# Kernel optimization log

Measured on AMD Instinct MI355X. Metric: run time of the kernel, lower is better.

Reference implementation:

```python
import jax, jax.numpy as jnp
import numpy as np
import math

B, T, D = 2, 2048, 1024
H, HD = 16, 64          # num_heads, head_dim = D // H
ROPE, BASE = 64, 10000.0  # rope covers full head dim
GLOBAL_IDS = jnp.array([2, 3, 4, 5, 6, 7], dtype=jnp.int32)


def setup_inputs() -> dict:
    key = jax.random.key(0)
    k1, k2, k3, k4 = jax.random.split(key, 4)
    x = jax.random.normal(k1, (B, T, D), dtype=jnp.float32)
    input_ids = jax.random.randint(k2, (B, T), 0, 1024, dtype=jnp.int32)
    W_qkv = jax.random.normal(k3, (3 * H * HD, D), dtype=jnp.float32) * 0.02
    b_qkv = jnp.zeros((3 * H * HD,), dtype=jnp.float32)
    W_out = jax.random.normal(k4, (D, H * HD), dtype=jnp.float32) * 0.02
    b_out = jnp.zeros((D,), dtype=jnp.float32)
    return {"x": x, "input_ids": input_ids, "W_qkv": W_qkv, "b_qkv": b_qkv,
            "W_out": W_out, "b_out": b_out}


def _apply_rotary(x, cos, sin):
    # x: [B,H,T,HD]; rope covers first ROPE dims (= full head here)
    x_rot, x_pass = x[..., :ROPE], x[..., ROPE:]
    half = ROPE // 2
    x1, x2 = x_rot[..., :half], x_rot[..., half:]
    x1n = x1 * cos - x2 * sin
    x2n = x1 * sin + x2 * cos
    return jnp.concatenate([x1n, x2n, x_pass], axis=-1)


def reference(x, input_ids, W_qkv, b_qkv, W_out, b_out):
    Bx, Tx, _ = x.shape
    qkv = x @ W_qkv.T + b_qkv                      # [B,T,3*H*HD]
    q, k, v = jnp.split(qkv, 3, axis=-1)
    def heads(t):
        return t.reshape(Bx, Tx, H, HD).transpose(0, 2, 1, 3)  # [B,H,T,HD]
    q, k, v = heads(q), heads(k), heads(v)

    # RoPE
    pos = jnp.arange(Tx, dtype=jnp.float32)
    inv_freq = 1.0 / (BASE ** (jnp.arange(0, ROPE, 2, dtype=jnp.float32) / ROPE))
    freqs = pos[:, None] * inv_freq[None, :]        # [T, ROPE//2]
    cos, sin = jnp.cos(freqs)[None, None], jnp.sin(freqs)[None, None]
    q = _apply_rotary(q, cos, sin)
    k = _apply_rotary(k, cos, sin)

    # causal mask OR global-query rows (BigBird-style)
    causal = jnp.tril(jnp.ones((Tx, Tx), dtype=bool))[None, None]   # [1,1,T,T]
    global_mask = jnp.isin(input_ids, GLOBAL_IDS)                    # [B,T]
    allow = causal | global_mask[:, None, :, None]                   # [B,1,T,T]

    scale = math.sqrt(HD)
    logits = jnp.einsum('bhqd,bhkd->bhqk', q, k) / scale
    neg = -jnp.finfo(logits.dtype).max
    logits = jnp.where(allow, logits, neg)
    attn = jax.nn.softmax(logits, axis=-1)
    out = jnp.einsum('bhqk,bhkd->bhqd', attn, v)
    out = out.transpose(0, 2, 1, 3).reshape(Bx, Tx, H * HD)
    return out @ W_out.T + b_out
```

## Files before the change

### kernel.cpp

```cpp
#include <hip/hip_runtime.h>
#include <math.h>

#define Bc 2
#define Tc 2048
#define Dc 1024
#define Hc 16
#define HDc 64

typedef __attribute__((ext_vector_type(8))) short bf16x8;
typedef __attribute__((ext_vector_type(4))) float f32x4;
typedef __attribute__((ext_vector_type(16))) float f32x16;

__device__ __forceinline__ unsigned short f2bf(float f) {
    union { float f; unsigned int u; } v; v.f = f;
    unsigned int r = (v.u + 0x7FFFu + ((v.u >> 16) & 1u)) >> 16;
    return (unsigned short)r;
}
__device__ __forceinline__ unsigned pack2bf(float a, float b) {
    unsigned au = __float_as_uint(a) + 0x8000u;
    unsigned bu = __float_as_uint(b) + 0x8000u;
    return __builtin_amdgcn_perm(bu, au, 0x07060302u);
}

__device__ __forceinline__ void gload_lds16(const unsigned short* g,
                                            unsigned short* l) {
    __builtin_amdgcn_global_load_lds(
        (const __attribute__((address_space(1))) unsigned int*)g,
        (__attribute__((address_space(3))) unsigned int*)l,
        16, 0, 0);
}

#define CEXP 0.1803368801111204f

__global__ __launch_bounds__(256) void convert_bf16(
    const float* __restrict__ x, const float* __restrict__ wqkv,
    const float* __restrict__ wout,
    unsigned short* __restrict__ xb, unsigned short* __restrict__ wqkvb,
    unsigned short* __restrict__ woutb, float2* __restrict__ ropeTab)
{
    const int gid = blockIdx.x * 256 + threadIdx.x;
    if (gid < Tc * 32) {
        const int t = gid >> 5, i = gid & 31;
        const float freq = exp2f((float)i * -0.4152410118609203f);
        const float ang = (float)t * freq;
        ropeTab[gid] = make_float2(cosf(ang), sinf(ang));
    }
    const int i = gid * 4;
    const float* src; unsigned short* dst; int off;
    if (i < 4194304)      { src = x;    dst = xb;    off = i; }
    else if (i < 7340032) { src = wqkv; dst = wqkvb; off = i - 4194304; }
    else                  { src = wout; dst = woutb; off = i - 7340032; }
    float4 v = *(const float4*)&src[off];
    ushort4 o;
    o.x = f2bf(v.x); o.y = f2bf(v.y); o.z = f2bf(v.z); o.w = f2bf(v.w);
    *(ushort4*)&dst[off] = o;
}

template <int MODE>
__global__ __launch_bounds__(256) void gemm_mfma(
    const unsigned short* __restrict__ A, const unsigned short* __restrict__ W,
    const float* __restrict__ bias, float* __restrict__ C,
    unsigned short* __restrict__ Qp, unsigned short* __restrict__ Kp,
    unsigned short* __restrict__ Vtp, const float2* __restrict__ ropeTab,
    int M, int N, int K)
{
    __shared__ unsigned short Apk[128 * 8 * 8];
    __shared__ unsigned short Bpk[128 * 8 * 8];

    const int tid = threadIdx.x;
    const int lane = tid & 63;
    const int wave = tid >> 6;
    const int quad = lane >> 4;
    const int c = lane & 15;
    const int wm = wave >> 1;
    const int wn = wave & 1;
    const int m0 = blockIdx.y * 128;
    const int n0 = blockIdx.x * 128;

    f32x4 acc[4][4];
#pragma unroll
    for (int mt = 0; mt < 4; mt++)
#pragma unroll
        for (int nt = 0; nt < 4; nt++) acc[mt][nt] = (f32x4){0.f, 0.f, 0.f, 0.f};

    const int lrow = lane >> 3;
    const int srcoct = (lane & 7) ^ lrow;

    for (int k0 = 0; k0 < K; k0 += 64) {
        __syncthreads();
#pragma unroll
        for (int i = 0; i < 4; i++) {
            const int r = wave * 32 + i * 8 + lrow;
            gload_lds16(&A[(size_t)(m0 + r) * K + k0 + srcoct * 8],
                        &Apk[(wave * 32 + i * 8) * 64]);
            gload_lds16(&W[(size_t)(n0 + r) * K + k0 + srcoct * 8],
                        &Bpk[(wave * 32 + i * 8) * 64]);
        }
        __syncthreads();
#pragma unroll
        for (int ko = 0; ko < 2; ko++) {
            bf16x8 af[4], bf[4];
#pragma unroll
            for (int mt = 0; mt < 4; mt++) {
                const int m = wm * 64 + mt * 16 + c;
                af[mt] = *(const bf16x8*)&Apk[(m * 8 + ((ko * 4 + quad) ^ (m & 7))) * 8];
            }
#pragma unroll
            for (int nt = 0; nt < 4; nt++) {
                const int n = wn * 64 + nt * 16 + c;
                bf[nt] = *(const bf16x8*)&Bpk[(n * 8 + ((ko * 4 + quad) ^ (n & 7))) * 8];
            }
#pragma unroll
            for (int mt = 0; mt < 4; mt++)
#pragma unroll
                for (int nt = 0; nt < 4; nt++)
                    acc[mt][nt] = __builtin_amdgcn_mfma_f32_16x16x32_bf16(
                        af[mt], bf[nt], acc[mt][nt], 0, 0, 0);
        }
    }

    if (MODE == 0) {
#pragma unroll
        for (int mt = 0; mt < 4; mt++) {
            const int m = m0 + wm * 64 + mt * 16 + quad * 4;
#pragma unroll
            for (int nt = 0; nt < 4; nt++) {
                const int n = n0 + wn * 64 + nt * 16 + c;
                const float bv = bias[n];
#pragma unroll
                for (int reg = 0; reg < 4; reg++)
                    C[(size_t)(m + reg) * N + n] = acc[mt][nt][reg] + bv;
            }
        }
    } else {
        const int n_wave = n0 + wn * 64;
        const int which = n_wave >> 10;
        const int h = (n_wave >> 6) & 15;
        const int b = m0 >> 11;
        const int t_base = (m0 & 2047) + wm * 64;

        __syncthreads();
        unsigned short* stg = ((wave < 2) ? Apk : Bpk) + (wave & 1) * 4096;

        if (which < 2) {
            unsigned short* dst = (which == 0) ? Qp : Kp;
#pragma unroll
            for (int mt = 0; mt < 4; mt++) {
#pragma unroll
                for (int nt = 0; nt < 2; nt++) {
                    const int i1 = nt * 16 + c;
                    const float bv1 = bias[n_wave + i1];
                    const float bv2 = bias[n_wave + 32 + i1];
#pragma unroll
                    for (int reg = 0; reg < 4; reg++) {
                        const int row = mt * 16 + quad * 4 + reg;
                        const float2 cs = ropeTab[(t_base + row) * 32 + i1];
                        const float x1 = acc[mt][nt][reg] + bv1;
                        const float x2 = acc[mt][nt + 2][reg] + bv2;
                        const int col2 = 32 + i1;
                        stg[(row * 8 + ((i1 >> 3) ^ (row & 7))) * 8 + (i1 & 7)] =
                            f2bf(x1 * cs.x - x2 * cs.y);
                        stg[(row * 8 + ((col2 >> 3) ^ (row & 7))) * 8 + (col2 & 7)] =
                            f2bf(x1 * cs.y + x2 * cs.x);
                    }
                }
            }
            const size_t obase = ((size_t)(b * Hc + h) * Tc + t_base) * HDc;
            const int oct = lane & 7;
#pragma unroll
            for (int k = 0; k < 8; k++) {
                const int f = lane * 8 + k * 512;
                const int row = f >> 6;
                bf16x8 vv = *(const bf16x8*)&stg[(row * 8 + (oct ^ (row & 7))) * 8];
                *(bf16x8*)&dst[obase + f] = vv;
            }
        } else {
#pragma unroll
            for (int mt = 0; mt < 4; mt++) {
#pragma unroll
                for (int nt = 0; nt < 4; nt++) {
                    const int d = nt * 16 + c;
                    const float bv = bias[n_wave + d];
#pragma unroll
                    for (int reg = 0; reg < 4; reg++) {
                        const int r = mt * 16 + quad * 4 + reg;
                        stg[(d * 8 + ((r >> 3) ^ (d & 7))) * 8 + (r & 7)] =
                            f2bf(acc[mt][nt][reg] + bv);
                    }
                }
            }
            const size_t vbase = (size_t)(b * Hc + h) * HDc * Tc;
            const int oct = lane & 7;
#pragma unroll
            for (int k = 0; k < 8; k++) {
                const int d = (lane >> 3) + k * 8;
                bf16x8 vv = *(const bf16x8*)&stg[(d * 8 + (oct ^ (d & 7))) * 8];
                *(bf16x8*)&Vtp[vbase + (size_t)d * Tc + t_base + oct * 8] = vv;
            }
        }
    }
}

__global__ __launch_bounds__(256) void attn_fused(
    const unsigned short* __restrict__ Q, const unsigned short* __restrict__ K,
    const unsigned short* __restrict__ Vt, const int* __restrict__ ids,
    unsigned short* __restrict__ AO)
{
    __shared__ float smem[8448];

    const int tid = threadIdx.x;
    const int lane = tid & 63;
    const int wave = tid >> 6;
    const int c32 = lane & 31;
    const int h = lane >> 5;
    const int blk = blockIdx.x;

    if (blk < 32) {
        int* s_list = (int*)smem;
        int* s_cnt = (int*)smem + 64;
        float* s_accm = smem + 128;
        float* s_lm = s_accm + 8192;

        const int bh = blk;
        const int b = bh >> 4;
        const int hd = bh & 15;
        const size_t qkbase = (size_t)bh * Tc * HDc;

        if (tid == 0) *s_cnt = 0;
        __syncthreads();
        for (int i = tid; i < Tc; i += 256) {
            int id = ids[b * Tc + i];
            if ((unsigned)(id - 2) <= 5u) {
                int p = atomicAdd(s_cnt, 1);
                if (p < 64) s_list[p] = i;
            }
        }
        __syncthreads();
        const int cnt = min(*s_cnt, 64);

        for (int pass = 0; pass * 32 < cnt; pass++) {
            const int slot = pass * 32 + c32;
            const int row = (slot < cnt) ? s_list[slot] : s_list[0];

            bf16x8 qf[4];
#pragma unroll
            for (int ko = 0; ko < 4; ko++)
                qf[ko] = *(const bf16x8*)&Q[qkbase + (size_t)row * HDc + ko * 16 + h * 8];

            f32x16 acc0 = {}, acc1 = {};
            float lacc = 0.0f;

            for (int it = wave; it < Tc / 64; it += 4) {
                const int t0 = it * 64;
                f32x16 s0 = {}, s1 = {};
#pragma unroll
                for (int ko = 0; ko < 4; ko++) {
                    const int koff = ko * 16 + h * 8;
                    bf16x8 kf0 = *(const bf16x8*)&K[qkbase + (size_t)(t0 + c32) * HDc + koff];
                    bf16x8 kf1 = *(const bf16x8*)&K[qkbase + (size_t)(t0 + 32 + c32) * HDc + koff];
                    s0 = __builtin_amdgcn_mfma_f32_32x32x16_bf16(kf0, qf[ko], s0, 0, 0, 0);
                    s1 = __builtin_amdgcn_mfma_f32_32x32x16_bf16(kf1, qf[ko], s1, 0, 0, 0);
                }
                float v[32];
#pragma unroll
                for (int r = 0; r < 16; r++) { v[r] = s0[r]; v[16 + r] = s1[r]; }
#pragma unroll
                for (int i = 0; i < 32; i++) v[i] = exp2f(v[i] * CEXP);
                unsigned pk[16];
#pragma unroll
                for (int i = 0; i < 16; i++) pk[i] = pack2bf(v[2 * i], v[2 * i + 1]);
#pragma unroll
                for (int st = 1; st < 32; st <<= 1)
#pragma unroll
                    for (int i = 0; i < 32; i += 2 * st) v[i] += v[i + st];
                lacc += v[0];
#pragma unroll
                for (int ko = 0; ko < 4; ko++) {
                    const int a = (ko >> 1) * 8 + (ko & 1) * 4;
                    unsigned keep0 = h ? pk[a + 2] : pk[a + 0];
                    unsigned keep1 = h ? pk[a + 3] : pk[a + 1];
                    unsigned send0 = h ? pk[a + 0] : pk[a + 2];
                    unsigned send1 = h ? pk[a + 1] : pk[a + 3];
                    unsigned recv0 = (unsigned)__shfl_xor((int)send0, 32);
                    unsigned recv1 = (unsigned)__shfl_xor((int)send1, 32);
                    union { bf16x8 v8; unsigned u[4]; } pf;
                    pf.u[0] = h ? recv0 : keep0;
                    pf.u[1] = h ? recv1 : keep1;
                    pf.u[2] = h ? keep0 : recv0;
                    pf.u[3] = h ? keep1 : recv1;
                    const int oct = ko * 2 + h;
                    bf16x8 vf0 = *(const bf16x8*)&Vt[qkbase + (size_t)c32 * Tc + t0 + oct * 8];
                    bf16x8 vf1 = *(const bf16x8*)&Vt[qkbase + (size_t)(32 + c32) * Tc + t0 + oct * 8];
                    acc0 = __builtin_amdgcn_mfma_f32_32x32x16_bf16(vf0, pf.v8, acc0, 0, 0, 0);
                    acc1 = __builtin_amdgcn_mfma_f32_32x32x16_bf16(vf1, pf.v8, acc1, 0, 0, 0);
                }
            }

            const float lfull = lacc + __shfl_xor(lacc, 32);
            if (h == 0) s_lm[wave * 32 + c32] = lfull;
#pragma unroll
            for (int r = 0; r < 16; r++) {
                const int d = (r & 3) + 8 * (r >> 2) + 4 * h;
                s_accm[(wave * 64 + d) * 32 + c32] = acc0[r];
                s_accm[(wave * 64 + 32 + d) * 32 + c32] = acc1[r];
            }
            __syncthreads();
            for (int i = tid; i < 2048; i += 256) {
                const int sl = i >> 6, d = i & 63;
                if (pass * 32 + sl < cnt) {
                    const float o = s_accm[(0 * 64 + d) * 32 + sl] + s_accm[(1 * 64 + d) * 32 + sl] +
                                    s_accm[(2 * 64 + d) * 32 + sl] + s_accm[(3 * 64 + d) * 32 + sl];
                    const float lt = s_lm[sl] + s_lm[32 + sl] + s_lm[64 + sl] + s_lm[96 + sl];
                    const int qrow = s_list[pass * 32 + sl];
                    AO[((size_t)(b * Tc + qrow)) * Dc + hd * HDc + d] = f2bf(o / lt);
                }
            }
            __syncthreads();
        }
        return;
    }

    unsigned short* KV = (unsigned short*)smem;

    const int idx = blk - 32;
    const int bh = idx & 31;
    const int b = bh >> 4;
    const int hd = bh & 15;
    const int qb = 15 - (idx >> 5);
    const int qb0 = qb * 128;
    const int wq0 = qb0 + wave * 32;
    const size_t qkbase = (size_t)bh * Tc * HDc;
    const int q = wq0 + c32;

    bf16x8 qf[4];
#pragma unroll
    for (int ko = 0; ko < 4; ko++)
        qf[ko] = *(const bf16x8*)&Q[qkbase + (size_t)q * HDc + ko * 16 + h * 8];

    const int myid = ids[b * Tc + q];
    const bool gr = ((unsigned)(myid - 2) <= 5u);

    f32x16 acc0 = {}, acc1 = {};
    float lacc = 0.0f;

    const int nIter = 2 * qb + 2;
    const int skey = tid >> 3;
    const int soct = tid & 7;

    bf16x8 kA0, kA1, vA0, vA1, kB0, kB1, vB0, vB1;

    auto loadT = [&](int t0, bf16x8& k0, bf16x8& k1, bf16x8& v0, bf16x8& v1) {
        const int r0 = skey, r1 = skey + 32;
        k0 = *(const bf16x8*)&K[qkbase + (size_t)(t0 + r0) * HDc + soct * 8];
        k1 = *(const bf16x8*)&K[qkbase + (size_t)(t0 + r1) * HDc + soct * 8];
        v0 = *(const bf16x8*)&Vt[qkbase + (size_t)r0 * Tc + t0 + soct * 8];
        v1 = *(const bf16x8*)&Vt[qkbase + (size_t)r1 * Tc + t0 + soct * 8];
    };
    auto writeT = [&](int buf, bf16x8 k0, bf16x8 k1, bf16x8 v0, bf16x8 v1) {
        const int r0 = skey, r1 = skey + 32;
        unsigned short* Kb = KV + buf * 4096;
        unsigned short* Vb = KV + 8192 + buf * 4096;
        *(bf16x8*)&Kb[(r0 * 8 + (soct ^ (r0 & 7))) * 8] = k0;
        *(bf16x8*)&Kb[(r1 * 8 + (soct ^ (r1 & 7))) * 8] = k1;
        *(bf16x8*)&Vb[(r0 * 8 + (soct ^ (r0 & 7))) * 8] = v0;
        *(bf16x8*)&Vb[(r1 * 8 + (soct ^ (r1 & 7))) * 8] = v1;
    };

    auto compute = [&](int buf, int t0) {
        if (t0 > wq0 + 31) return;
        const unsigned short* Kb = KV + buf * 4096;
        const unsigned short* Vb = KV + 8192 + buf * 4096;

        f32x16 s0 = {}, s1 = {};
#pragma unroll
        for (int ko = 0; ko < 4; ko++) {
            const int oct = ko * 2 + h;
            const int k0i = c32;
            const int k1i = 32 + c32;
            bf16x8 kf0 = *(const bf16x8*)&Kb[(k0i * 8 + (oct ^ (k0i & 7))) * 8];
            bf16x8 kf1 = *(const bf16x8*)&Kb[(k1i * 8 + (oct ^ (k1i & 7))) * 8];
            s0 = __builtin_amdgcn_mfma_f32_32x32x16_bf16(kf0, qf[ko], s0, 0, 0, 0);
            s1 = __builtin_amdgcn_mfma_f32_32x32x16_bf16(kf1, qf[ko], s1, 0, 0, 0);
        }

        float v[32];
#pragma unroll
        for (int r = 0; r < 16; r++) { v[r] = s0[r]; v[16 + r] = s1[r]; }
#pragma unroll
        for (int i = 0; i < 32; i++) v[i] = exp2f(v[i] * CEXP);

        const bool needMask = (t0 + 63 > wq0);
        if (needMask) {
            const int thr = wq0 + c32 - t0 - 4 * h;
#pragma unroll
            for (int kt = 0; kt < 2; kt++)
#pragma unroll
                for (int r = 0; r < 16; r++) {
                    const int ckr = kt * 32 + (r & 3) + 8 * (r >> 2);
                    v[kt * 16 + r] = (ckr <= thr) ? v[kt * 16 + r] : 0.0f;
                }
        }

        unsigned pk[16];
#pragma unroll
        for (int i = 0; i < 16; i++) pk[i] = pack2bf(v[2 * i], v[2 * i + 1]);

#pragma unroll
        for (int st = 1; st < 32; st <<= 1)
#pragma unroll
            for (int i = 0; i < 32; i += 2 * st) v[i] += v[i + st];
        lacc += v[0];

#pragma unroll
        for (int ko = 0; ko < 4; ko++) {
            const int a = (ko >> 1) * 8 + (ko & 1) * 4;
            unsigned keep0 = h ? pk[a + 2] : pk[a + 0];
            unsigned keep1 = h ? pk[a + 3] : pk[a + 1];
            unsigned send0 = h ? pk[a + 0] : pk[a + 2];
            unsigned send1 = h ? pk[a + 1] : pk[a + 3];
            unsigned recv0 = (unsigned)__shfl_xor((int)send0, 32);
            unsigned recv1 = (unsigned)__shfl_xor((int)send1, 32);
            union { bf16x8 v8; unsigned u[4]; } pf;
            pf.u[0] = h ? recv0 : keep0;
            pf.u[1] = h ? recv1 : keep1;
            pf.u[2] = h ? keep0 : recv0;
            pf.u[3] = h ? keep1 : recv1;
            const int oct = ko * 2 + h;
            const int d0 = c32, d1 = 32 + c32;
            bf16x8 vf0 = *(const bf16x8*)&Vb[(d0 * 8 + (oct ^ (d0 & 7))) * 8];
            bf16x8 vf1 = *(const bf16x8*)&Vb[(d1 * 8 + (oct ^ (d1 & 7))) * 8];
            acc0 = __builtin_amdgcn_mfma_f32_32x32x16_bf16(vf0, pf.v8, acc0, 0, 0, 0);
            acc1 = __builtin_amdgcn_mfma_f32_32x32x16_bf16(vf1, pf.v8, acc1, 0, 0, 0);
        }
    };

    loadT(0, kA0, kA1, vA0, vA1);
    writeT(0, kA0, kA1, vA0, vA1);
    for (int it = 0; ; it += 2) {
        __syncthreads();
        const bool p1 = (it + 1) < nIter;
        if (p1) loadT((it + 1) * 64, kB0, kB1, vB0, vB1);
        compute(0, it * 64);
        if (!p1) break;
        writeT(1, kB0, kB1, vB0, vB1);
        __syncthreads();
        const bool p2 = (it + 2) < nIter;
        if (p2) loadT((it + 2) * 64, kA0, kA1, vA0, vA1);
        compute(1, (it + 1) * 64);
        if (!p2) break;
        writeT(0, kA0, kA1, vA0, vA1);
    }

    const float l = lacc + __shfl_xor(lacc, 32);
    if (!gr) {
        const float inv = 1.0f / l;
        unsigned short* dst = &AO[((size_t)(b * Tc + q)) * Dc + hd * HDc];
#pragma unroll
        for (int i = 0; i < 8; i++) {
            const int r = 2 * i;
            const int d = (r & 3) + 8 * (r >> 2) + 4 * h;
            *(unsigned*)&dst[d]      = pack2bf(acc0[r] * inv, acc0[r + 1] * inv);
            *(unsigned*)&dst[32 + d] = pack2bf(acc1[r] * inv, acc1[r + 1] * inv);
        }
    }
}

extern "C" void kernel_launch(void* const* d_in, const int* in_sizes, int n_in,
                              void* d_out, int out_size, void* d_ws, size_t ws_size,
                              hipStream_t stream)
{
    const float* x    = (const float*)d_in[0];
    const int*   ids  = (const int*)d_in[1];
    const float* Wqkv = (const float*)d_in[2];
    const float* bqkv = (const float*)d_in[3];
    const float* Wout = (const float*)d_in[4];
    const float* bout = (const float*)d_in[5];
    float* out = (float*)d_out;

    const size_t TEN = (size_t)Bc * Hc * Tc * HDc;
    unsigned short* xb    = (unsigned short*)d_ws;
    unsigned short* wqkvb = xb + 4194304;
    unsigned short* woutb = wqkvb + 3145728;
    float2* ropeTab       = (float2*)(woutb + 1048576);
    unsigned short* Qb    = (unsigned short*)(ropeTab + 65536);
    unsigned short* Kb    = Qb + TEN;
    unsigned short* Vtb   = Kb + TEN;
    unsigned short* AOb   = Vtb + TEN;

    convert_bf16<<<8192, 256, 0, stream>>>(x, Wqkv, Wout, xb, wqkvb, woutb,
                                           ropeTab);
    dim3 g1(3072 / 128, 4096 / 128);
    gemm_mfma<1><<<g1, 256, 0, stream>>>(xb, wqkvb, bqkv, nullptr,
                                         Qb, Kb, Vtb, ropeTab, 4096, 3072, 1024);
    attn_fused<<<544, 256, 0, stream>>>(Qb, Kb, Vtb, ids, AOb);
    dim3 g4(1024 / 128, 4096 / 128);
    gemm_mfma<0><<<g4, 256, 0, stream>>>(AOb, woutb, bout, out,
                                         nullptr, nullptr, nullptr, nullptr,
                                         4096, 1024, 1024);
}
```

Measured before the change: 202.7 us.

## Split attention into 64-row query blocks with key-split wave pairs and direct LDS loads

The causal attention grid now uses 64-row query blocks instead of 128, giving 1024 blocks, ordered to interleave long and short blocks for load balance. Within each block two wave pairs process alternate key tiles, and their partial accumulators are merged through shared memory at the end. K/V staging switches from register loads followed by LDS writes to direct global-to-LDS loads, and launch bounds request 4 blocks per CU. The cost is an extra merge step, the loss of overlap between loading and computing within a block, and register pressure from the occupancy hint.

Result: no change. 200.7 us (-1.0%).

```diff
diff --git a/kernel.cpp b/kernel.cpp
--- a/kernel.cpp
+++ b/kernel.cpp
@@ -201,12 +201,12 @@
     }
 }
 
-__global__ __launch_bounds__(256) void attn_fused(
+__global__ __launch_bounds__(256, 4) void attn_fused(
     const unsigned short* __restrict__ Q, const unsigned short* __restrict__ K,
     const unsigned short* __restrict__ Vt, const int* __restrict__ ids,
     unsigned short* __restrict__ AO)
 {
-    __shared__ float smem[8448];
+    __shared__ __align__(16) float smem[8448];
 
     const int tid = threadIdx.x;
     const int lane = tid & 63;
@@ -321,14 +321,21 @@
     }
 
     unsigned short* KV = (unsigned short*)smem;
+    unsigned short* Ke = KV;
+    unsigned short* Ko = KV + 4096;
+    unsigned short* Ve = KV + 8192;
+    unsigned short* Vo = KV + 12288;
 
     const int idx = blk - 32;
-    const int bh = idx & 31;
+    const int bh = (idx & 7) + 8 * ((idx >> 3) & 3);
     const int b = bh >> 4;
     const int hd = bh & 15;
-    const int qb = 15 - (idx >> 5);
-    const int qb0 = qb * 128;
-    const int wq0 = qb0 + wave * 32;
+    const int w = idx >> 5;
+    const int u = w & 7, tq = w >> 3;
+    const int j = (tq == 0) ? u : (tq == 1) ? 31 - u : (tq == 2) ? 8 + u : 23 - u;
+    const int qb0 = j * 64;
+    const int nT = j + 1;
+    const int wq0 = qb0 + (wave & 1) * 32;
     const size_t qkbase = (size_t)bh * Tc * HDc;
     const int q = wq0 + c32;
 
@@ -343,34 +350,30 @@
     f32x16 acc0 = {}, acc1 = {};
     float lacc = 0.0f;
 
-    const int nIter = 2 * qb + 2;
-    const int skey = tid >> 3;
-    const int soct = tid & 7;
-
-    bf16x8 kA0, kA1, vA0, vA1, kB0, kB1, vB0, vB1;
-
-    auto loadT = [&](int t0, bf16x8& k0, bf16x8& k1, bf16x8& v0, bf16x8& v1) {
-        const int r0 = skey, r1 = skey + 32;
-        k0 = *(const bf16x8*)&K[qkbase + (size_t)(t0 + r0) * HDc + soct * 8];
-        k1 = *(const bf16x8*)&K[qkbase + (size_t)(t0 + r1) * HDc + soct * 8];
-        v0 = *(const bf16x8*)&Vt[qkbase + (size_t)r0 * Tc + t0 + soct * 8];
-        v1 = *(const bf16x8*)&Vt[qkbase + (size_t)r1 * Tc + t0 + soct * 8];
+    const int lrow = lane >> 3;
+    const int srcoct = (lane & 7) ^ lrow;
+    const int jb = wave * 2;
+
+    auto stageK = [&](int t0, unsigned short* buf) {
+#pragma unroll
+        for (int i = 0; i < 2; i++) {
+            const int jj = jb + i;
+            const int row = jj * 8 + lrow;
+            gload_lds16(&K[qkbase + (size_t)(t0 + row) * HDc + srcoct * 8],
+                        &buf[jj * 512]);
+        }
     };
-    auto writeT = [&](int buf, bf16x8 k0, bf16x8 k1, bf16x8 v0, bf16x8 v1) {
-        const int r0 = skey, r1 = skey + 32;
-        unsigned short* Kb = KV + buf * 4096;
-        unsigned short* Vb = KV + 8192 + buf * 4096;
-        *(bf16x8*)&Kb[(r0 * 8 + (soct ^ (r0 & 7))) * 8] = k0;
-        *(bf16x8*)&Kb[(r1 * 8 + (soct ^ (r1 & 7))) * 8] = k1;
-        *(bf16x8*)&Vb[(r0 * 8 + (soct ^ (r0 & 7))) * 8] = v0;
-        *(bf16x8*)&Vb[(r1 * 8 + (soct ^ (r1 & 7))) * 8] = v1;
+    auto stageV = [&](int t0, unsigned short* buf) {
+#pragma unroll
+        for (int i = 0; i < 2; i++) {
+            const int jj = jb + i;
+            const int d = jj * 8 + lrow;
+            gload_lds16(&Vt[qkbase + (size_t)d * Tc + t0 + srcoct * 8],
+                        &buf[jj * 512]);
+        }
     };
 
-    auto compute = [&](int buf, int t0) {
-        if (t0 > wq0 + 31) return;
-        const unsigned short* Kb = KV + buf * 4096;
-        const unsigned short* Vb = KV + 8192 + buf * 4096;
-
+    auto computeT = [&](int t0, const unsigned short* Kb, const unsigned short* Vb) {
         f32x16 s0 = {}, s1 = {};
 #pragma unroll
         for (int ko = 0; ko < 4; ko++) {
@@ -434,22 +437,38 @@
         }
     };
 
-    loadT(0, kA0, kA1, vA0, vA1);
-    writeT(0, kA0, kA1, vA0, vA1);
-    for (int it = 0; ; it += 2) {
-        __syncthreads();
-        const bool p1 = (it + 1) < nIter;
-        if (p1) loadT((it + 1) * 64, kB0, kB1, vB0, vB1);
-        compute(0, it * 64);
-        if (!p1) break;
-        writeT(1, kB0, kB1, vB0, vB1);
-        __syncthreads();
-        const bool p2 = (it + 2) < nIter;
-        if (p2) loadT((it + 2) * 64, kA0, kA1, vA0, vA1);
-        compute(1, (it + 1) * 64);
-        if (!p2) break;
-        writeT(0, kA0, kA1, vA0, vA1);
-    }
+    for (int tp = 0; tp < nT; tp += 2) {
+        __syncthreads();
+        stageK(tp * 64, Ke);
+        stageV(tp * 64, Ve);
+        const bool has2 = (tp + 1) < nT;
+        if (has2) {
+            stageK((tp + 1) * 64, Ko);
+            stageV((tp + 1) * 64, Vo);
+        }
+        __syncthreads();
+        if ((wave >> 1) == 0) computeT(tp * 64, Ke, Ve);
+        else if (has2) computeT((tp + 1) * 64, Ko, Vo);
+    }
+
+    __syncthreads();
+    float* mrg = smem + (wave & 1) * 2176;
+    if (wave >= 2) {
+#pragma unroll
+        for (int r = 0; r < 16; r++) {
+            mrg[r * 64 + lane] = acc0[r];
+            mrg[(16 + r) * 64 + lane] = acc1[r];
+        }
+        mrg[2048 + lane] = lacc;
+    }
+    __syncthreads();
+    if (wave >= 2) return;
+#pragma unroll
+    for (int r = 0; r < 16; r++) {
+        acc0[r] += mrg[r * 64 + lane];
+        acc1[r] += mrg[(16 + r) * 64 + lane];
+    }
+    lacc += mrg[2048 + lane];
 
     const float l = lacc + __shfl_xor(lacc, 32);
     if (!gr) {
@@ -492,7 +511,7 @@
     dim3 g1(3072 / 128, 4096 / 128);
     gemm_mfma<1><<<g1, 256, 0, stream>>>(xb, wqkvb, bqkv, nullptr,
                                          Qb, Kb, Vtb, ropeTab, 4096, 3072, 1024);
-    attn_fused<<<544, 256, 0, stream>>>(Qb, Kb, Vtb, ids, AOb);
+    attn_fused<<<1056, 256, 0, stream>>>(Qb, Kb, Vtb, ids, AOb);
     dim3 g4(1024 / 128, 4096 / 128);
     gemm_mfma<0><<<g4, 256, 0, stream>>>(AOb, woutb, bout, out,
                                          nullptr, nullptr, nullptr, nullptr,
```
